# Kernel optimization log

Measured on AMD Instinct MI355X. Metric: run time of the kernel, lower is better.

## Reference

```python
import jax, jax.numpy as jnp
import numpy as np
import math

B, H, M, L, D = 4, 8, 512, 2048, 64   # batch, heads, block len, span, head dim
RAMP = 64                              # adapt_span_len (soft-mask ramp size)


def setup_inputs() -> dict:
    key = jax.random.key(0)
    ks = jax.random.split(key, 5)
    BH = B * H
    KL = M + L
    return {
        "query": jax.random.normal(ks[0], (BH, M, D), jnp.float32),
        "key_": jax.random.normal(ks[1], (BH, KL, D), jnp.float32),
        "value": jax.random.normal(ks[2], (BH, KL, D), jnp.float32),
        "key_pe": jax.random.normal(ks[3], (1, D, L), jnp.float32) * 0.02,
        "current_val": jax.random.uniform(ks[4], (H, 1, 1), jnp.float32, minval=0.3, maxval=0.9),
    }


def reference(query, key_, value, key_pe, current_val):
    BH, Mq, Dh = query.shape
    KL = key_.shape[1]
    Lw = KL - Mq  # attention span
    nb = BH // current_val.shape[0]  # batch size (heads folded into leading dim)

    # full scores then unskew: band[b, i, j] = scores[b, i, i + j]
    scores = jnp.einsum('bmd,bnd->bmn', query, key_)              # (BH, M, M+L)
    rows = jnp.arange(Mq)[:, None]                                # (M, 1)
    band_idx = rows + jnp.arange(Lw)[None, :]                     # (M, L)
    attn = scores[:, rows, band_idx]                              # (BH, M, L)

    # relative position bias, scale, softmax
    attn = attn + jnp.einsum('bmd,dl->bml', query, key_pe[0])
    attn = attn / math.sqrt(Dh)
    attn = jax.nn.softmax(attn, axis=-1)

    # adaptive span soft mask (per head) + renormalization
    template = jnp.arange(1 - Lw, 1, dtype=attn.dtype)            # (L,) = linspace(1-L, 0, L)
    mask = jnp.clip((template + current_val * Lw) / RAMP + 1.0, 0.0, 1.0)  # (H, 1, L)
    attn4 = attn.reshape(nb, -1, Mq, Lw) * mask[None]             # (B, H, M, L)
    attn4 = attn4 / (attn4.sum(-1, keepdims=True) + 1e-8)
    attn = attn4.reshape(BH, Mq, Lw)

    # skew back to (BH, M, M+L) and contract with values
    skewed = jnp.zeros((BH, Mq, KL), attn.dtype).at[:, rows, band_idx].set(attn)
    out = jnp.einsum('bmn,bnd->bmd', skewed, value)               # (BH, M, D)
    return out
```

## Files before the change

### kernel.cpp

```cpp
#include <hip/hip_runtime.h>
#include <math.h>

typedef _Float16 half_t;
typedef _Float16 half8 __attribute__((ext_vector_type(8)));
typedef _Float16 half4 __attribute__((ext_vector_type(4)));
typedef _Float16 half2v __attribute__((ext_vector_type(2)));
typedef float f32x2 __attribute__((ext_vector_type(2)));
typedef float f32x4 __attribute__((ext_vector_type(4)));
typedef float f32x16 __attribute__((ext_vector_type(16)));
typedef unsigned int uint4v __attribute__((ext_vector_type(4)));

#define MFMA_S(a, b, c) __builtin_amdgcn_mfma_f32_32x32x16_f16((a), (b), (c), 0, 0, 0)

static constexpr int kM  = 512;
static constexpr int kD  = 64;
static constexpr int kKL = 2560;
static constexpr int kL  = 2048;
static constexpr int WS_VC  = 0;
static constexpr int WS_PET = WS_VC + 5242880;
static constexpr size_t WS_ZP_B = 10747904;
static constexpr size_t WS_PO_B = WS_ZP_B + 262144;

__global__ __launch_bounds__(256) void prep_tr(const float* __restrict__ v,
    const float* __restrict__ pe, half_t* __restrict__ ws) {
  __shared__ float ls[64 * 72];
  const int b = blockIdx.x, t = threadIdx.x;
  const bool isV = (b < 1280);
  int bh = 0, kt = 0, b3 = 0;
  const float* src; int sstride;
  if (isV) {
    bh = b / 40; kt = b % 40;
    src = v + (size_t)(bh * 2560 + kt * 64) * 64; sstride = 64;
  } else {
    b3 = b - 1280;
    src = pe + (size_t)b3 * 64; sstride = 2048;
  }
  const int rr = t >> 4, cq = (t & 15) * 4;
#pragma unroll
  for (int p = 0; p < 4; ++p) {
    const float4 x = *(const float4*)(src + (size_t)(p * 16 + rr) * sstride + cq);
    *(float4*)(ls + (p * 16 + rr) * 72 + cq) = x;
  }
  __syncthreads();
  const int oc = t >> 2, ch = t & 3;
  half_t tmp[16];
#pragma unroll
  for (int i2 = 0; i2 < 16; ++i2) tmp[i2] = (half_t)ls[(ch * 16 + i2) * 72 + oc];
  half_t* o;
  if (isV) {
    o = ws + WS_VC + (size_t)bh * 163840 + ((kt << 1) + (ch >> 1)) * 2048 + oc * 32 + ((ch & 1) << 4);
  } else {
    o = ws + WS_PET + ((size_t)b3 * 64 + oc) * 64 + ch * 16;
  }
  ((int4*)o)[0] = ((int4*)tmp)[0];
  ((int4*)o)[1] = ((int4*)tmp)[1];
}

__global__ __launch_bounds__(256, 2) void attn_kernel(
    const float* __restrict__ qg, const float* __restrict__ kg,
    const half_t* __restrict__ ws, const float* __restrict__ cvp,
    float* __restrict__ po, float* __restrict__ zp) {

  __shared__ __align__(16) char smem[53248];
  half_t* lsh = (half_t*)smem;

  const int tid  = threadIdx.x;
  const int lane = tid & 63;
  const int w    = tid >> 6;
  const int c32  = lane & 31;
  const int h    = lane >> 5;

  const int id = blockIdx.x;
  const int bh = ((id & 7) << 2) | (id >> 7);
  const int mid = (id >> 3) & 15;
  const int mb = mid & 3, sp = mid >> 2;
  const int m0 = mb << 7;
  const int g0 = sp * 17;

  const float cvl = cvp[bh & 7] * 2048.0f - 2047.0f;
  const float cvO = cvl * 0.015625f + 1.0f;

  const float*  kbF = kg + (size_t)bh * (kKL * kD);
  const half_t* vcb = ws + WS_VC + (size_t)bh * (kKL * kD);
  const half_t* pet = ws + WS_PET;

  const float QS = 0.125f * 1.4426950408889634f;
  const float* qrowF = qg + (size_t)(bh * kM + m0 + 32 * w + c32) * kD;
  half8 bq[4];
#pragma unroll
  for (int t = 0; t < 4; ++t) {
    const float4 qa = *(const float4*)(qrowF + t * 16 + h * 8);
    const float4 qb = *(const float4*)(qrowF + t * 16 + h * 8 + 4);
    bq[t] = half8{ (half_t)(qa.x * QS), (half_t)(qa.y * QS),
                   (half_t)(qa.z * QS), (half_t)(qa.w * QS),
                   (half_t)(qb.x * QS), (half_t)(qb.y * QS),
                   (half_t)(qb.z * QS), (half_t)(qb.w * QS) };
  }

  float* stfF = (float*)(smem + 19456) + w * 2112 + c32 * 66;

  float4 stgKa, stgKb; int4 stgV;
  auto issueKV = [&](int gg) {
    const int r = tid >> 3, seg = tid & 7;
    const int krow = m0 + (gg << 5) + r;
    const float* kp = kbF + (size_t)krow * kD + seg * 8;
    stgKa = *(const float4*)kp;
    stgKb = *(const float4*)(kp + 4);
    const int vch = (m0 >> 5) + gg;
    stgV = *(const int4*)(vcb + (size_t)vch * 2048 + tid * 8);
  };
  auto commitKV = [&](int gg) {
    const int sK = (gg & 1) * 2304;
    const int sV = 4608 + (gg & 1) * 2560;
    const int r = tid >> 3, seg = tid & 7;
    half_t tk[8];
    tk[0] = (half_t)stgKa.x; tk[1] = (half_t)stgKa.y;
    tk[2] = (half_t)stgKa.z; tk[3] = (half_t)stgKa.w;
    tk[4] = (half_t)stgKb.x; tk[5] = (half_t)stgKb.y;
    tk[6] = (half_t)stgKb.z; tk[7] = (half_t)stgKb.w;
    *(int4*)(lsh + sK + r * 72 + seg * 8) = *(int4*)tk;
    const int d = tid >> 2, ks = (tid & 3) * 8;
    *(int4*)(lsh + sV + d * 40 + ks) = stgV;
  };

  auto petLoad = [&](int wb, half8* p) {
    int l = wb + c32; l = l < 0 ? 0 : (l > kL - 1 ? kL - 1 : l);
    const half_t* pp = pet + (size_t)l * kD;
#pragma unroll
    for (int t = 0; t < 4; ++t) p[t] = *(const half8*)(pp + t * 16 + h * 8);
  };
  auto peMFMA = [&](const half8* p) -> f32x16 {
    f32x16 a = {};
#pragma unroll
    for (int t = 0; t < 4; ++t) a = MFMA_S(p[t], bq[t], a);
    return a;
  };
  auto stripWrite = [&](int wb, const f32x16& a) {
    const int allone  = (wb >= 0) && (wb + 31 <= kL - 1) && (wb + cvl >= 0.0f);
    const int allzero = (wb > kL - 1) || (wb + 31 < 0) || ((float)(wb + 31) + cvl <= -64.0f);
#pragma unroll
    for (int reg = 0; reg < 16; ++reg) {
      const int lr = (reg & 3) + 8 * (reg >> 2) + 4 * h;
      const int l  = wb + lr;
      float bl;
      if (allzero) bl = -HUGE_VALF;
      else if (allone) bl = a[reg];
      else {
        const float mk = fminf(fmaxf((float)l * 0.015625f + cvO, 0.0f), 1.0f);
        const float lg = __builtin_amdgcn_logf(mk);
        bl = ((unsigned)l < (unsigned)kL) ? a[reg] + lg : -HUGE_VALF;
      }
      stfF[(l + c32) & 63] = bl;
    }
  };

  issueKV(g0);
  const int B0 = (g0 << 5) - 32 * w;
  {
    half8 pq[4];
    petLoad(B0 - 32, pq); stripWrite(B0 - 32, peMFMA(pq));
    petLoad(B0,      pq); stripWrite(B0,      peMFMA(pq));
  }
  commitKV(g0);
  __syncthreads();

  float zmc = 0.0f;
  f32x16 o0 = {}, o1 = {};

  half8 pp[4];
  for (int t = 0; t < 17; ++t) {
    const int g = g0 + t;
    const bool more = (t < 16);
    const int B = (g << 5) - 32 * w;
    if (more) {
      issueKV(g + 1);
      petLoad(B + 32, pp);
    }

    const int sK = (g & 1) * 2304;
    const int sV = 4608 + (g & 1) * 2560;

    f32x16 s;
#pragma unroll
    for (int q = 0; q < 4; ++q) {
      const int base = (B + 8 * q + 4 * h) & 63;
      const f32x2 lo = *(const f32x2*)(stfF + base);
      const f32x2 hi = *(const f32x2*)(stfF + base + 2);
      s[4 * q + 0] = lo.x; s[4 * q + 1] = lo.y;
      s[4 * q + 2] = hi.x; s[4 * q + 3] = hi.y;
    }

    half8 ak[4];
#pragma unroll
    for (int kt = 0; kt < 4; ++kt)
      ak[kt] = *(const half8*)(lsh + sK + c32 * 72 + kt * 16 + h * 8);

    half8 av[2][2];
#pragma unroll
    for (int dh = 0; dh < 2; ++dh)
#pragma unroll
      for (int kt = 0; kt < 2; ++kt)
        av[dh][kt] = *(const half8*)(lsh + sV + (32 * dh + c32) * 40 + kt * 16 + h * 8);

#pragma unroll
    for (int kt = 0; kt < 4; ++kt) s = MFMA_S(ak[kt], bq[kt], s);

    float pm[16];
#pragma unroll
    for (int reg = 0; reg < 16; ++reg) pm[reg] = __builtin_amdgcn_exp2f(s[reg]);
    {
      const float t0 = (pm[0] + pm[1]) + (pm[2] + pm[3]);
      const float t1 = (pm[4] + pm[5]) + (pm[6] + pm[7]);
      const float t2 = (pm[8] + pm[9]) + (pm[10] + pm[11]);
      const float t3 = (pm[12] + pm[13]) + (pm[14] + pm[15]);
      zmc += (t0 + t1) + (t2 + t3);
    }
    unsigned Wp[8];
#pragma unroll
    for (int q = 0; q < 8; ++q)
      Wp[q] = __builtin_bit_cast(unsigned,
                __builtin_amdgcn_cvt_pkrtz(pm[2 * q], pm[2 * q + 1]));
    const auto r0 = __builtin_amdgcn_permlane32_swap(Wp[0], Wp[2], false, false);
    const auto r1 = __builtin_amdgcn_permlane32_swap(Wp[1], Wp[3], false, false);
    const auto r2 = __builtin_amdgcn_permlane32_swap(Wp[4], Wp[6], false, false);
    const auto r3 = __builtin_amdgcn_permlane32_swap(Wp[5], Wp[7], false, false);
    const uint4v u0 = { (unsigned)r0[0], (unsigned)r1[0], (unsigned)r0[1], (unsigned)r1[1] };
    const uint4v u1 = { (unsigned)r2[0], (unsigned)r3[0], (unsigned)r2[1], (unsigned)r3[1] };
    const half8 pb0 = __builtin_bit_cast(half8, u0);
    const half8 pb1 = __builtin_bit_cast(half8, u1);

    o0 = MFMA_S(av[0][0], pb0, o0);
    o0 = MFMA_S(av[0][1], pb1, o0);
    o1 = MFMA_S(av[1][0], pb0, o1);
    o1 = MFMA_S(av[1][1], pb1, o1);

    if (more) {
      stripWrite(B + 32, peMFMA(pp));
      commitKV(g + 1);
    }
    __syncthreads();
  }

  float* Ow = (float*)smem + (size_t)w * 2176;
#pragma unroll
  for (int q = 0; q < 4; ++q) {
    *(f32x4*)(Ow + c32 * 68 + 0  + 8 * q + 4 * h) =
        f32x4{o0[q * 4], o0[q * 4 + 1], o0[q * 4 + 2], o0[q * 4 + 3]};
    *(f32x4*)(Ow + c32 * 68 + 32 + 8 * q + 4 * h) =
        f32x4{o1[q * 4], o1[q * 4 + 1], o1[q * 4 + 2], o1[q * 4 + 3]};
  }
  zmc += __shfl_xor(zmc, 32);
  const int rowbase = bh * kM + m0 + 32 * w;
  if (lane < 32) zp[(size_t)sp * 16384 + rowbase + c32] = zmc;
  __syncthreads();
  float* pob = po + ((size_t)sp * 16384 + rowbase) * 64;
#pragma unroll
  for (int u = 0; u < 8; ++u) {
    const int row = u * 4 + (lane >> 4);
    const int d4 = (lane & 15) << 2;
    *(f32x4*)(pob + (size_t)row * 64 + d4) = *(const f32x4*)(Ow + row * 68 + d4);
  }
}

__global__ __launch_bounds__(256) void norm_kernel(const float* __restrict__ zp,
    const float* __restrict__ po, float* __restrict__ out) {
  const int i = blockIdx.x * 256 + threadIdx.x;
  const int row = i >> 4, d4 = (i & 15) << 2;
  const float z = zp[row] + zp[16384 + row] + zp[32768 + row] + zp[49152 + row];
  const float inv = 1.0f / (z + 1e-20f);
  f32x4 a = *(const f32x4*)(po + (size_t)row * 64 + d4);
  const f32x4 b = *(const f32x4*)(po + 1048576u + (size_t)row * 64 + d4);
  const f32x4 c = *(const f32x4*)(po + 2097152u + (size_t)row * 64 + d4);
  const f32x4 d = *(const f32x4*)(po + 3145728u + (size_t)row * 64 + d4);
  a = a + b + c + d;
  *(f32x4*)(out + (size_t)row * 64 + d4) = a * inv;
}

extern "C" void kernel_launch(void* const* d_in, const int* in_sizes, int n_in,
                              void* d_out, int out_size, void* d_ws, size_t ws_size,
                              hipStream_t stream) {
  (void)in_sizes; (void)n_in; (void)out_size; (void)ws_size;
  const float* q  = (const float*)d_in[0];
  const float* k  = (const float*)d_in[1];
  const float* v  = (const float*)d_in[2];
  const float* pe = (const float*)d_in[3];
  const float* cv = (const float*)d_in[4];
  half_t* ws = (half_t*)d_ws;
  float* out = (float*)d_out;
  float* zp = (float*)((char*)d_ws + WS_ZP_B);
  float* po = (float*)((char*)d_ws + WS_PO_B);

  prep_tr<<<1312, 256, 0, stream>>>(v, pe, ws);
  attn_kernel<<<512, 256, 0, stream>>>(q, k, ws, cv, po, zp);
  norm_kernel<<<1024, 256, 0, stream>>>(zp, po, out);
}
```

Measured before the change: 130.5 us.

## Deepen K prefetch to two tiles ahead with quad-buffered LDS

```diff
diff --git a/kernel.cpp b/kernel.cpp
--- a/kernel.cpp
+++ b/kernel.cpp
@@ -61,7 +61,7 @@
     const half_t* __restrict__ ws, const float* __restrict__ cvp,
     float* __restrict__ po, float* __restrict__ zp) {
 
-  __shared__ __align__(16) char smem[53248];
+  __shared__ __align__(16) char smem[62464];
   half_t* lsh = (half_t*)smem;
 
   const int tid  = threadIdx.x;
@@ -97,33 +97,38 @@
                    (half_t)(qb.z * QS), (half_t)(qb.w * QS) };
   }
 
-  float* stfF = (float*)(smem + 19456) + w * 2112 + c32 * 66;
-
-  float4 stgKa, stgKb; int4 stgV;
-  auto issueKV = [&](int gg) {
+  float* stfF = (float*)(smem + 28672) + w * 2112 + c32 * 66;
+
+  auto issueK = [&](int gg, float4& a, float4& b) {
     const int r = tid >> 3, seg = tid & 7;
     const int krow = m0 + (gg << 5) + r;
     const float* kp = kbF + (size_t)krow * kD + seg * 8;
-    stgKa = *(const float4*)kp;
-    stgKb = *(const float4*)(kp + 4);
+    a = *(const float4*)kp;
+    b = *(const float4*)(kp + 4);
+  };
+  auto commitK = [&](int gg, const float4& a, const float4& b) {
+    half_t* kbf = lsh + (gg & 3) * 2304;
+    const int r = tid >> 3, seg = tid & 7;
+    half_t tk[8];
+    tk[0] = (half_t)a.x; tk[1] = (half_t)a.y;
+    tk[2] = (half_t)a.z; tk[3] = (half_t)a.w;
+    tk[4] = (half_t)b.x; tk[5] = (half_t)b.y;
+    tk[6] = (half_t)b.z; tk[7] = (half_t)b.w;
+    *(int4*)(kbf + r * 72 + seg * 8) = *(int4*)tk;
+  };
+
+  int4 stgV;
+  auto issueV = [&](int gg) {
     const int vch = (m0 >> 5) + gg;
     stgV = *(const int4*)(vcb + (size_t)vch * 2048 + tid * 8);
   };
-  auto commitKV = [&](int gg) {
-    const int sK = (gg & 1) * 2304;
-    const int sV = 4608 + (gg & 1) * 2560;
-    const int r = tid >> 3, seg = tid & 7;
-    half_t tk[8];
-    tk[0] = (half_t)stgKa.x; tk[1] = (half_t)stgKa.y;
-    tk[2] = (half_t)stgKa.z; tk[3] = (half_t)stgKa.w;
-    tk[4] = (half_t)stgKb.x; tk[5] = (half_t)stgKb.y;
-    tk[6] = (half_t)stgKb.z; tk[7] = (half_t)stgKb.w;
-    *(int4*)(lsh + sK + r * 72 + seg * 8) = *(int4*)tk;
+  auto commitV = [&](int gg) {
+    half_t* vbf = lsh + 9216 + (gg & 1) * 2560;
     const int d = tid >> 2, ks = (tid & 3) * 8;
-    *(int4*)(lsh + sV + d * 40 + ks) = stgV;
-  };
-
-  auto petLoad = [&](int wb, half8* p) {
+    *(int4*)(vbf + d * 40 + ks) = stgV;
+  };
+
+  auto petL = [&](int wb, half8* p) {
     int l = wb + c32; l = l < 0 ? 0 : (l > kL - 1 ? kL - 1 : l);
     const half_t* pp = pet + (size_t)l * kD;
 #pragma unroll
@@ -154,31 +159,12 @@
     }
   };
 
-  issueKV(g0);
-  const int B0 = (g0 << 5) - 32 * w;
-  {
-    half8 pq[4];
-    petLoad(B0 - 32, pq); stripWrite(B0 - 32, peMFMA(pq));
-    petLoad(B0,      pq); stripWrite(B0,      peMFMA(pq));
-  }
-  commitKV(g0);
-  __syncthreads();
-
   float zmc = 0.0f;
   f32x16 o0 = {}, o1 = {};
 
-  half8 pp[4];
-  for (int t = 0; t < 17; ++t) {
-    const int g = g0 + t;
-    const bool more = (t < 16);
-    const int B = (g << 5) - 32 * w;
-    if (more) {
-      issueKV(g + 1);
-      petLoad(B + 32, pp);
-    }
-
-    const int sK = (g & 1) * 2304;
-    const int sV = 4608 + (g & 1) * 2560;
+  auto doStep = [&](int g, int B) {
+    half_t* kbf = lsh + (g & 3) * 2304;
+    half_t* vbf = lsh + 9216 + (g & 1) * 2560;
 
     f32x16 s;
 #pragma unroll
@@ -193,14 +179,14 @@
     half8 ak[4];
 #pragma unroll
     for (int kt = 0; kt < 4; ++kt)
-      ak[kt] = *(const half8*)(lsh + sK + c32 * 72 + kt * 16 + h * 8);
+      ak[kt] = *(const half8*)(kbf + c32 * 72 + kt * 16 + h * 8);
 
     half8 av[2][2];
 #pragma unroll
     for (int dh = 0; dh < 2; ++dh)
 #pragma unroll
       for (int kt = 0; kt < 2; ++kt)
-        av[dh][kt] = *(const half8*)(lsh + sV + (32 * dh + c32) * 40 + kt * 16 + h * 8);
+        av[dh][kt] = *(const half8*)(vbf + (32 * dh + c32) * 40 + kt * 16 + h * 8);
 
 #pragma unroll
     for (int kt = 0; kt < 4; ++kt) s = MFMA_S(ak[kt], bq[kt], s);
@@ -233,14 +219,54 @@
     o0 = MFMA_S(av[0][1], pb1, o0);
     o1 = MFMA_S(av[1][0], pb0, o1);
     o1 = MFMA_S(av[1][1], pb1, o1);
-
-    if (more) {
-      stripWrite(B + 32, peMFMA(pp));
-      commitKV(g + 1);
+  };
+
+  float4 sKa0, sKb0, sKa1, sKb1;
+  half8 pp0[4], pp1[4];
+  const int B0 = (g0 << 5) - 32 * w;
+  issueK(g0, sKa0, sKb0);
+  issueK(g0 + 1, sKa1, sKb1);
+  issueV(g0);
+  {
+    half8 pq[4];
+    petL(B0 - 32, pq); stripWrite(B0 - 32, peMFMA(pq));
+    petL(B0,      pq); stripWrite(B0,      peMFMA(pq));
+  }
+  commitK(g0, sKa0, sKb0);
+  commitV(g0);
+  petL(B0 + 32, pp1);
+  __syncthreads();
+
+  for (int p = 0; p < 8; ++p) {
+    const int t = 2 * p;
+    const int g = g0 + t;
+    const int B = (g << 5) - 32 * w;
+
+    issueK(g + 2, sKa0, sKb0);
+    issueV(g + 1);
+    petL(B + 64, pp0);
+    doStep(g, B);
+    commitK(g + 1, sKa1, sKb1);
+    commitV(g + 1);
+    stripWrite(B + 32, peMFMA(pp1));
+    __syncthreads();
+
+    const int g2 = g + 1;
+    const int B2 = B + 32;
+    if (p < 7) {
+      issueK(g2 + 2, sKa1, sKb1);
+      petL(B2 + 64, pp1);
     }
+    issueV(g2 + 1);
+    doStep(g2, B2);
+    commitK(g2 + 1, sKa0, sKb0);
+    commitV(g2 + 1);
+    stripWrite(B2 + 32, peMFMA(pp0));
     __syncthreads();
   }
-
+  doStep(g0 + 16, (g0 + 16) * 32 - 32 * w);
+
+  __syncthreads();
   float* Ow = (float*)smem + (size_t)w * 2176;
 #pragma unroll
   for (int q = 0; q < 4; ++q) {
```

After: 131.5 us. No clear change (+0.7%).
